# Kernel tuning notes

Hardware: AMD Instinct MI355X
Metric: run time of the kernel (lower is better)

## Reference

```python
import jax, jax.numpy as jnp
import numpy as np

B, Q, K, F, H, D = 2, 4096, 4096, 512, 8, 64

def setup_inputs() -> dict:
    key = jax.random.key(0)
    ks = jax.random.split(key, 6)
    s = 1.0 / np.sqrt(F)
    return {
        "inputs_q": jax.random.normal(ks[0], (B, Q, F), dtype=jnp.float32),
        "inputs_kv": jax.random.normal(ks[1], (B, K, F), dtype=jnp.float32),
        "Wq": jax.random.normal(ks[2], (F, H, D), dtype=jnp.float32) * s,
        "Wk": jax.random.normal(ks[3], (F, H, D), dtype=jnp.float32) * s,
        "Wv": jax.random.normal(ks[4], (F, H, D), dtype=jnp.float32) * s,
        "Wo": jax.random.normal(ks[5], (H, D, F), dtype=jnp.float32) * (1.0 / np.sqrt(H * D)),
    }

def reference(inputs_q, inputs_kv, Wq, Wk, Wv, Wo):
    # QKV projections (DenseGeneral, no bias): [B, L, F] -> [B, L, H, D]
    q = jnp.einsum("bqf,fhd->bqhd", inputs_q, Wq)
    k = jnp.einsum("bkf,fhd->bkhd", inputs_kv, Wk)
    v = jnp.einsum("bkf,fhd->bkhd", inputs_kv, Wv)
    # Explicit attention matrix [B, H, Q, K] as in the original module
    logits = jnp.einsum("bqhd,bkhd->bhqk", q, k)
    attn = jax.nn.softmax(logits, axis=-1)
    out = jnp.einsum("bhqk,bkhd->bqhd", attn, v)
    # Output projection over (heads, head_dim): [B, Q, H, D] -> [B, Q, F]
    return jnp.einsum("bqhd,hdf->bqf", out, Wo)
```

## Files before the change

### kernel.cpp

```cpp
#include <hip/hip_runtime.h>
#include <hip/hip_bf16.h>

typedef short bf16x8 __attribute__((ext_vector_type(8)));
typedef _Float16 f16;
typedef f16 f16x8 __attribute__((ext_vector_type(8)));
typedef float f32x4 __attribute__((ext_vector_type(4)));
typedef unsigned short u16;
typedef u16 u16x8 __attribute__((ext_vector_type(8)));
typedef unsigned int u32;
typedef u32 u32x2 __attribute__((ext_vector_type(2)));

#define B_  2
#define L_  4096
#define F_  512
#define H_  8
#define D_  64
#define M_  8192
#define NSPL 2
#define KHALF (L_ / NSPL)

#define LOG2E 1.442695041f

__device__ inline u16 f2bf(float f) {
    union { float f; unsigned u; } v; v.f = f;
    unsigned r = v.u + 0x7fff + ((v.u >> 16) & 1);
    return (u16)(r >> 16);
}
__device__ inline u16 f2h(float f) {
    union { f16 h; u16 u; } v; v.h = (f16)f;
    return v.u;
}
__device__ inline float h2f(u16 u) {
    union { u16 u; f16 h; } v; v.u = u;
    return (float)v.h;
}

__global__ __launch_bounds__(256) void wt_kernel(
    const float* __restrict__ Wq, const float* __restrict__ Wk,
    const float* __restrict__ Wv, const float* __restrict__ Wo,
    u16* __restrict__ Tq, u16* __restrict__ Tk,
    u16* __restrict__ Tv, u16* __restrict__ To) {
    __shared__ float t[32][33];
    const int z = blockIdx.z;
    const float* in = (z == 0) ? Wq : (z == 1) ? Wk : (z == 2) ? Wv : Wo;
    u16* out = (z == 0) ? Tq : (z == 1) ? Tk : (z == 2) ? Tv : To;
    int k0 = blockIdx.y * 32, n0 = blockIdx.x * 32;
    int c = threadIdx.x & 31, r8 = threadIdx.x >> 5;
#pragma unroll
    for (int i = 0; i < 4; ++i) {
        int r = r8 * 4 + i;
        t[r][c] = in[(size_t)(k0 + r) * F_ + n0 + c];
    }
    __syncthreads();
#pragma unroll
    for (int i = 0; i < 4; ++i) {
        int r = r8 * 4 + i;
        out[(size_t)(n0 + r) * F_ + k0 + c] = f2h(t[c][r]);
    }
}

__global__ __launch_bounds__(256, 3) void proj_kernel(
    const float* __restrict__ Xq, const float* __restrict__ Xkv,
    const u16* __restrict__ Wqt, const u16* __restrict__ Wkt,
    const u16* __restrict__ Wvt,
    u16* __restrict__ Qw, u16* __restrict__ Kw, u16* __restrict__ Vw) {
    __shared__ u16 Ah[128][72];
    __shared__ u16 B1[64][72];
    __shared__ u16 B2[64][72];
    const int tid = threadIdx.x;
    const int w = tid >> 6, lane = tid & 63, lx = lane & 15, quad = lane >> 4;
    const int m0 = blockIdx.y * 128, n0 = blockIdx.x * 64;
    const bool isKV = (blockIdx.z == 1);
    const float* A = isKV ? Xkv : Xq;
    const u16* W1 = isKV ? Wkt : Wqt;

    float4 apre[8];
    u16x8 b1p[2], b2p[2];

    auto load_ab = [&](int k0) {
#pragma unroll
        for (int it = 0; it < 4; ++it) {
            int slot = tid + it * 256, r = slot >> 3, g = (slot & 7) * 8;
            apre[2 * it]     = *(const float4*)(A + (size_t)(m0 + r) * F_ + k0 + g);
            apre[2 * it + 1] = *(const float4*)(A + (size_t)(m0 + r) * F_ + k0 + g + 4);
        }
#pragma unroll
        for (int it = 0; it < 2; ++it) {
            int slot = tid + it * 256, r = slot >> 3, g = (slot & 7) * 8;
            b1p[it] = *(const u16x8*)(W1 + (size_t)(n0 + r) * F_ + k0 + g);
            if (isKV)
                b2p[it] = *(const u16x8*)(Wvt + (size_t)(n0 + r) * F_ + k0 + g);
        }
    };
    auto write_ab = [&]() {
#pragma unroll
        for (int it = 0; it < 4; ++it) {
            int slot = tid + it * 256, r = slot >> 3, g = (slot & 7) * 8;
            float4 f0 = apre[2 * it], f1 = apre[2 * it + 1];
            u16 th[8] = {f2h(f0.x), f2h(f0.y), f2h(f0.z), f2h(f0.w),
                         f2h(f1.x), f2h(f1.y), f2h(f1.z), f2h(f1.w)};
            *(u16x8*)&Ah[r][g] = *(u16x8*)th;
        }
#pragma unroll
        for (int it = 0; it < 2; ++it) {
            int slot = tid + it * 256, r = slot >> 3, g = (slot & 7) * 8;
            *(u16x8*)&B1[r][g] = b1p[it];
            if (isKV) *(u16x8*)&B2[r][g] = b2p[it];
        }
    };

    f32x4 acc1[2][4] = {}, acc2[2][4] = {};

    load_ab(0);
    write_ab();
    __syncthreads();
    load_ab(64);

    for (int k0 = 0; k0 < F_; k0 += 64) {
#pragma unroll
        for (int ks = 0; ks < 2; ++ks) {
            f16x8 af[2];
#pragma unroll
            for (int mf = 0; mf < 2; ++mf)
                af[mf] = *(const f16x8*)&Ah[w * 32 + mf * 16 + lx][ks * 32 + quad * 8];
#pragma unroll
            for (int nt = 0; nt < 4; ++nt) {
                f16x8 b1 = *(const f16x8*)&B1[nt * 16 + lx][ks * 32 + quad * 8];
#pragma unroll
                for (int mf = 0; mf < 2; ++mf)
                    acc1[mf][nt] = __builtin_amdgcn_mfma_f32_16x16x32_f16(af[mf], b1, acc1[mf][nt], 0, 0, 0);
                if (isKV) {
                    f16x8 b2 = *(const f16x8*)&B2[nt * 16 + lx][ks * 32 + quad * 8];
#pragma unroll
                    for (int mf = 0; mf < 2; ++mf)
                        acc2[mf][nt] = __builtin_amdgcn_mfma_f32_16x16x32_f16(af[mf], b2, acc2[mf][nt], 0, 0, 0);
                }
            }
        }
        if (k0 < F_ - 64) {
            __syncthreads();
            write_ab();
            __syncthreads();
            if (k0 < F_ - 128) load_ab(k0 + 128);
        }
    }

    const int h = n0 >> 6;
    const float scl = isKV ? 1.0f : LOG2E;
    u16* C1 = isKV ? Kw : Qw;
#pragma unroll
    for (int mf = 0; mf < 2; ++mf)
#pragma unroll
        for (int nt = 0; nt < 4; ++nt)
#pragma unroll
            for (int i = 0; i < 4; ++i) {
                int m = m0 + w * 32 + mf * 16 + quad * 4 + i;
                int b = m >> 12, l = m & 4095;
                int d = nt * 16 + lx;
                C1[((size_t)(b * H_ + h) * L_ + l) * D_ + d] = f2h(acc1[mf][nt][i] * scl);
            }
    if (isKV) {
        __syncthreads();
#pragma unroll
        for (int mf = 0; mf < 2; ++mf)
#pragma unroll
            for (int nt = 0; nt < 4; ++nt)
#pragma unroll
                for (int i = 0; i < 4; ++i)
                    Ah[w * 32 + mf * 16 + quad * 4 + i][nt * 16 + lx] = f2bf(acc2[mf][nt][i]);
        __syncthreads();
        int d = tid >> 2, seg = (tid & 3) * 32;
        int b = m0 >> 12;
        u16 tmp[32];
#pragma unroll
        for (int j = 0; j < 32; ++j) tmp[j] = Ah[seg + j][d];
        size_t base = ((size_t)(b * H_ + h) * D_ + d) * L_ + (m0 & 4095) + seg;
#pragma unroll
        for (int c = 0; c < 4; ++c)
            *(u16x8*)(Vw + base + c * 8) = *(u16x8*)&tmp[c * 8];
    }
}

__global__ __launch_bounds__(256) void out_gemm(const u16* __restrict__ A16,
                                                const u16* __restrict__ Wt,
                                                float* __restrict__ Cf) {
    __shared__ u16 As[128][72];
    __shared__ u16 Bs[64][72];
    const int tid = threadIdx.x;
    const int w = tid >> 6, lane = tid & 63, lx = lane & 15, quad = lane >> 4;
    const int m0 = blockIdx.y * 128, n0 = blockIdx.x * 64;

    u16x8 a16p[4];
    u16x8 bp[2];

    auto load_ab = [&](int k0) {
#pragma unroll
        for (int it = 0; it < 4; ++it) {
            int slot = tid + it * 256, r = slot >> 3, g = (slot & 7) * 8;
            a16p[it] = *(const u16x8*)(A16 + (size_t)(m0 + r) * F_ + k0 + g);
        }
#pragma unroll
        for (int it = 0; it < 2; ++it) {
            int slot = tid + it * 256, r = slot >> 3, g = (slot & 7) * 8;
            bp[it] = *(const u16x8*)(Wt + (size_t)(n0 + r) * F_ + k0 + g);
        }
    };
    auto write_ab = [&]() {
#pragma unroll
        for (int it = 0; it < 4; ++it) {
            int slot = tid + it * 256, r = slot >> 3, g = (slot & 7) * 8;
            *(u16x8*)&As[r][g] = a16p[it];
        }
#pragma unroll
        for (int it = 0; it < 2; ++it) {
            int slot = tid + it * 256, r = slot >> 3, g = (slot & 7) * 8;
            *(u16x8*)&Bs[r][g] = bp[it];
        }
    };

    f32x4 acc[2][4] = {};

    load_ab(0);
    write_ab();
    __syncthreads();
    load_ab(64);

    for (int k0 = 0; k0 < F_; k0 += 64) {
#pragma unroll
        for (int ks = 0; ks < 2; ++ks) {
            f16x8 af[2];
#pragma unroll
            for (int mf = 0; mf < 2; ++mf)
                af[mf] = *(const f16x8*)&As[w * 32 + mf * 16 + lx][ks * 32 + quad * 8];
#pragma unroll
            for (int nt = 0; nt < 4; ++nt) {
                f16x8 bf = *(const f16x8*)&Bs[nt * 16 + lx][ks * 32 + quad * 8];
#pragma unroll
                for (int mf = 0; mf < 2; ++mf)
                    acc[mf][nt] = __builtin_amdgcn_mfma_f32_16x16x32_f16(af[mf], bf, acc[mf][nt], 0, 0, 0);
            }
        }
        if (k0 < F_ - 64) {
            __syncthreads();
            write_ab();
            __syncthreads();
            if (k0 < F_ - 128) load_ab(k0 + 128);
        }
    }

#pragma unroll
    for (int mf = 0; mf < 2; ++mf)
#pragma unroll
        for (int nt = 0; nt < 4; ++nt)
#pragma unroll
            for (int i = 0; i < 4; ++i) {
                int m = m0 + w * 32 + mf * 16 + quad * 4 + i;
                int n = n0 + nt * 16 + lx;
                Cf[(size_t)m * F_ + n] = acc[mf][nt][i];
            }
}

__global__ __launch_bounds__(256, 4) void flash_mfma(
    const u16* __restrict__ Qg, const u16* __restrict__ Kg,
    const u16* __restrict__ Vtg, u16* __restrict__ On, float* __restrict__ Ls) {
    __shared__ u16 Ks[64][72];
    __shared__ u16 Vs[64][72];

    const int tid = threadIdx.x;
    const int w = tid >> 6, lane = tid & 63, lx = lane & 15, quad = lane >> 4;

    const int x = blockIdx.x;
    const int t = x >> 3;
    const int hh = t >> 6;
    const int s = (t >> 5) & 1;
    const int bh = (x & 7) * 2 + hh;
    const int q0 = (t & 31) * 128;

    const u16* Qp = Qg + ((size_t)bh * L_ + q0) * D_;
    const u16* Kp = Kg + (size_t)bh * L_ * D_ + (size_t)(s * KHALF) * D_;
    const u16* Vp = Vtg + (size_t)bh * D_ * L_ + s * KHALF;

    f16x8 qreg[2][2];
#pragma unroll
    for (int qf = 0; qf < 2; ++qf)
#pragma unroll
        for (int ks = 0; ks < 2; ++ks)
            qreg[qf][ks] = *(const f16x8*)(Qp + (size_t)(w * 32 + qf * 16 + lx) * D_ +
                                           ks * 32 + quad * 8);

    u16x8 kp[2], vp[2];
    auto load_kv = [&](int kt) {
#pragma unroll
        for (int it = 0; it < 2; ++it) {
            int slot = tid + it * 256, r = slot >> 3, g = (slot & 7) * 8;
            kp[it] = *(const u16x8*)(Kp + (size_t)(kt * 64 + r) * D_ + g);
            vp[it] = *(const u16x8*)(Vp + (size_t)r * L_ + kt * 64 + g);
        }
    };
    auto write_kv = [&]() {
#pragma unroll
        for (int it = 0; it < 2; ++it) {
            int slot = tid + it * 256, r = slot >> 3, g = (slot & 7) * 8;
            *(u16x8*)&Ks[r][g] = kp[it];
            *(u16x8*)&Vs[r][g] = vp[it];
        }
    };

    const bf16x8 vone = {0x3F80, 0x3F80, 0x3F80, 0x3F80,
                         0x3F80, 0x3F80, 0x3F80, 0x3F80};
    f32x4 o[2][4] = {};
    f32x4 osum[2] = {};

    load_kv(0);
    write_kv();
    __syncthreads();
    load_kv(1);

    const int NT = KHALF / 64;
    for (int kt = 0; kt < NT; ++kt) {
        f32x4 sv[4][2] = {};
#pragma unroll
        for (int ks = 0; ks < 2; ++ks) {
#pragma unroll
            for (int nt = 0; nt < 4; ++nt) {
                f16x8 ak = *(const f16x8*)&Ks[nt * 16 + lx][ks * 32 + quad * 8];
#pragma unroll
                for (int qf = 0; qf < 2; ++qf)
                    sv[nt][qf] = __builtin_amdgcn_mfma_f32_16x16x32_f16(ak, qreg[qf][ks], sv[nt][qf], 0, 0, 0);
            }
        }

        u32 pu[4][2], pw[4][2];
#pragma unroll
        for (int nt = 0; nt < 4; ++nt)
#pragma unroll
            for (int qf = 0; qf < 2; ++qf) {
                u32 ub[4];
#pragma unroll
                for (int i = 0; i < 4; ++i)
                    ub[i] = __float_as_uint(__builtin_amdgcn_exp2f(sv[nt][qf][i]));
                pu[nt][qf] = __builtin_amdgcn_perm(ub[1], ub[0], 0x07060302u);
                pw[nt][qf] = __builtin_amdgcn_perm(ub[3], ub[2], 0x07060302u);
            }

        bf16x8 ap[2][2];
#pragma unroll
        for (int ks = 0; ks < 2; ++ks)
#pragma unroll
            for (int qf = 0; qf < 2; ++qf) {
                u32x2 r  = __builtin_amdgcn_permlane32_swap(pu[2 * ks][qf], pu[2 * ks + 1][qf], false, false);
                u32x2 r2 = __builtin_amdgcn_permlane16_swap(r[0], r[1], false, false);
                u32x2 t  = __builtin_amdgcn_permlane32_swap(pw[2 * ks][qf], pw[2 * ks + 1][qf], false, false);
                u32x2 t2 = __builtin_amdgcn_permlane16_swap(t[0], t[1], false, false);
                union { u32 d[4]; bf16x8 h; } cvt;
                cvt.d[0] = r2[0];
                cvt.d[1] = t2[0];
                cvt.d[2] = r2[1];
                cvt.d[3] = t2[1];
                ap[ks][qf] = cvt.h;
            }

#pragma unroll
        for (int ks = 0; ks < 2; ++ks) {
#pragma unroll
            for (int qf = 0; qf < 2; ++qf)
                osum[qf] = __builtin_amdgcn_mfma_f32_16x16x32_bf16(ap[ks][qf], vone, osum[qf], 0, 0, 0);
#pragma unroll
            for (int nt = 0; nt < 4; ++nt) {
                bf16x8 bv = *(const bf16x8*)&Vs[nt * 16 + lx][ks * 32 + quad * 8];
#pragma unroll
                for (int qf = 0; qf < 2; ++qf)
                    o[qf][nt] = __builtin_amdgcn_mfma_f32_16x16x32_bf16(ap[ks][qf], bv, o[qf][nt], 0, 0, 0);
            }
        }

        if (kt < NT - 1) {
            __syncthreads();
            write_kv();
            __syncthreads();
            if (kt < NT - 2) load_kv(kt + 2);
        }
    }

    const int b = bh >> 3, h = bh & 7;
    u16* Op = On + (size_t)s * M_ * F_;
#pragma unroll
    for (int qf = 0; qf < 2; ++qf) {
        float linv[4];
#pragma unroll
        for (int i = 0; i < 4; ++i) linv[i] = 1.f / osum[qf][i];
#pragma unroll
        for (int nt = 0; nt < 4; ++nt)
#pragma unroll
            for (int i = 0; i < 4; ++i) {
                int l = q0 + w * 32 + qf * 16 + quad * 4 + i;
                Op[((size_t)b * L_ + l) * (H_ * D_) + h * D_ + nt * 16 + lx] =
                    f2h(o[qf][nt][i] * linv[i]);
            }
        if (lx == 0) {
            float* lp = Ls + ((size_t)s * (B_ * H_) + bh) * L_ +
                        q0 + w * 32 + qf * 16 + quad * 4;
#pragma unroll
            for (int i = 0; i < 4; ++i) lp[i] = osum[qf][i];
        }
    }
}

__global__ __launch_bounds__(256) void reduce_kernel(
    const u16* __restrict__ On, const float* __restrict__ Ls,
    u16* __restrict__ Ow) {
    int gid = blockIdx.x * 256 + threadIdx.x;
    size_t off = (size_t)gid * 8;
    int row = gid >> 3;
    int b = row >> 15, rem = row & 32767;
    int l = rem >> 3, h = rem & 7;
    int lidx = ((b * H_ + h) << 12) + l;
    float l1 = Ls[lidx], l2 = Ls[B_ * H_ * L_ + lidx];
    float w1 = l1 / (l1 + l2), w2 = 1.f - w1;
    u16x8 a = *(const u16x8*)(On + off);
    u16x8 c = *(const u16x8*)(On + (size_t)M_ * F_ + off);
    u16 r[8];
#pragma unroll
    for (int j = 0; j < 8; ++j)
        r[j] = f2h(w1 * h2f(a[j]) + w2 * h2f(c[j]));
    *(u16x8*)(Ow + off) = *(u16x8*)r;
}

extern "C" void kernel_launch(void* const* d_in, const int* in_sizes, int n_in,
                              void* d_out, int out_size, void* d_ws, size_t ws_size,
                              hipStream_t stream)
{
    const float* Xq  = (const float*)d_in[0];
    const float* Xkv = (const float*)d_in[1];
    const float* Wq  = (const float*)d_in[2];
    const float* Wk  = (const float*)d_in[3];
    const float* Wv  = (const float*)d_in[4];
    const float* Wo  = (const float*)d_in[5];
    float* out = (float*)d_out;

    u16* ws  = (u16*)d_ws;
    const size_t MF = (size_t)M_ * F_;
    const size_t FF = (size_t)F_ * F_;
    u16* Wqt = ws;
    u16* Wkt = Wqt + FF;
    u16* Wvt = Wkt + FF;
    u16* Wot = Wvt + FF;
    u16* Qw  = Wot + FF;
    u16* Kw  = Qw + MF;
    u16* Vw  = Kw + MF;
    u16* On  = Vw + MF;
    float* Ls = (float*)(On + 2 * MF);
    u16* Ow  = Qw;

    wt_kernel<<<dim3(16, 16, 4), 256, 0, stream>>>(Wq, Wk, Wv, Wo,
                                                   Wqt, Wkt, Wvt, Wot);

    proj_kernel<<<dim3(8, 64, 2), 256, 0, stream>>>(Xq, Xkv, Wqt, Wkt, Wvt,
                                                    Qw, Kw, Vw);

    flash_mfma<<<dim3(1024), 256, 0, stream>>>(Qw, Kw, Vw, On, Ls);

    reduce_kernel<<<dim3((int)(MF / 8 / 256)), 256, 0, stream>>>(On, Ls, Ow);

    out_gemm<<<dim3(8, 64), 256, 0, stream>>>(Ow, Wot, out);
}
```

Baseline: 232.8 us.

## Double-buffer K/V in LDS, double query tile per block, split key tile into halves

The flash kernel now processes 256 queries per block (64 per wave) so each K/V tile loaded into LDS is reused across twice as many queries, and the grid is halved accordingly. K/V tiles are double-buffered in shared memory, so the next tile is written during compute and only one barrier per iteration remains. The 64-key tile is processed in two 32-key halves so exp/permute work on one half can interleave with MFMAs, with s_setprio raised around the PV MFMA blocks. This raises register and LDS use (launch bounds drop to 2 blocks per CU), trading occupancy for reuse and fewer syncs.

Measured after the change: 215.9 us. 1.08x faster.

```diff
diff --git a/kernel.cpp b/kernel.cpp
--- a/kernel.cpp
+++ b/kernel.cpp
@@ -260,32 +260,32 @@
             }
 }
 
-__global__ __launch_bounds__(256, 4) void flash_mfma(
+__global__ __launch_bounds__(256, 2) void flash_mfma(
     const u16* __restrict__ Qg, const u16* __restrict__ Kg,
     const u16* __restrict__ Vtg, u16* __restrict__ On, float* __restrict__ Ls) {
-    __shared__ u16 Ks[64][72];
-    __shared__ u16 Vs[64][72];
+    __shared__ u16 Ks[2][64][72];
+    __shared__ u16 Vs[2][64][72];
 
     const int tid = threadIdx.x;
     const int w = tid >> 6, lane = tid & 63, lx = lane & 15, quad = lane >> 4;
 
     const int x = blockIdx.x;
     const int t = x >> 3;
-    const int hh = t >> 6;
-    const int s = (t >> 5) & 1;
+    const int hh = t >> 5;
+    const int s = (t >> 4) & 1;
     const int bh = (x & 7) * 2 + hh;
-    const int q0 = (t & 31) * 128;
+    const int q0 = (t & 15) * 256;
 
     const u16* Qp = Qg + ((size_t)bh * L_ + q0) * D_;
     const u16* Kp = Kg + (size_t)bh * L_ * D_ + (size_t)(s * KHALF) * D_;
     const u16* Vp = Vtg + (size_t)bh * D_ * L_ + s * KHALF;
 
-    f16x8 qreg[2][2];
-#pragma unroll
-    for (int qf = 0; qf < 2; ++qf)
+    f16x8 qreg[4][2];
+#pragma unroll
+    for (int qf = 0; qf < 4; ++qf)
 #pragma unroll
         for (int ks = 0; ks < 2; ++ks)
-            qreg[qf][ks] = *(const f16x8*)(Qp + (size_t)(w * 32 + qf * 16 + lx) * D_ +
+            qreg[qf][ks] = *(const f16x8*)(Qp + (size_t)(w * 64 + qf * 16 + lx) * D_ +
                                            ks * 32 + quad * 8);
 
     u16x8 kp[2], vp[2];
@@ -297,95 +297,141 @@
             vp[it] = *(const u16x8*)(Vp + (size_t)r * L_ + kt * 64 + g);
         }
     };
-    auto write_kv = [&]() {
+    auto write_kv = [&](int p) {
 #pragma unroll
         for (int it = 0; it < 2; ++it) {
             int slot = tid + it * 256, r = slot >> 3, g = (slot & 7) * 8;
-            *(u16x8*)&Ks[r][g] = kp[it];
-            *(u16x8*)&Vs[r][g] = vp[it];
+            *(u16x8*)&Ks[p][r][g] = kp[it];
+            *(u16x8*)&Vs[p][r][g] = vp[it];
         }
     };
 
     const bf16x8 vone = {0x3F80, 0x3F80, 0x3F80, 0x3F80,
                          0x3F80, 0x3F80, 0x3F80, 0x3F80};
-    f32x4 o[2][4] = {};
-    f32x4 osum[2] = {};
+    f32x4 o[4][4] = {};
+    f32x4 osum[4] = {};
 
     load_kv(0);
-    write_kv();
+    write_kv(0);
     __syncthreads();
     load_kv(1);
 
     const int NT = KHALF / 64;
     for (int kt = 0; kt < NT; ++kt) {
-        f32x4 sv[4][2] = {};
-#pragma unroll
-        for (int ks = 0; ks < 2; ++ks) {
-#pragma unroll
-            for (int nt = 0; nt < 4; ++nt) {
-                f16x8 ak = *(const f16x8*)&Ks[nt * 16 + lx][ks * 32 + quad * 8];
-#pragma unroll
-                for (int qf = 0; qf < 2; ++qf)
+        const int p = kt & 1;
+
+        f32x4 sv[2][4] = {};
+#pragma unroll
+        for (int ks = 0; ks < 2; ++ks)
+#pragma unroll
+            for (int nt = 0; nt < 2; ++nt) {
+                f16x8 ak = *(const f16x8*)&Ks[p][nt * 16 + lx][ks * 32 + quad * 8];
+#pragma unroll
+                for (int qf = 0; qf < 4; ++qf)
                     sv[nt][qf] = __builtin_amdgcn_mfma_f32_16x16x32_f16(ak, qreg[qf][ks], sv[nt][qf], 0, 0, 0);
             }
-        }
-
-        u32 pu[4][2], pw[4][2];
-#pragma unroll
-        for (int nt = 0; nt < 4; ++nt)
-#pragma unroll
-            for (int qf = 0; qf < 2; ++qf) {
+
+        if (kt < NT - 1) write_kv(p ^ 1);
+
+        bf16x8 ap0[4];
+#pragma unroll
+        for (int qf = 0; qf < 4; ++qf) {
+            u32 pu[2], pw[2];
+#pragma unroll
+            for (int nt = 0; nt < 2; ++nt) {
                 u32 ub[4];
 #pragma unroll
                 for (int i = 0; i < 4; ++i)
                     ub[i] = __float_as_uint(__builtin_amdgcn_exp2f(sv[nt][qf][i]));
-                pu[nt][qf] = __builtin_amdgcn_perm(ub[1], ub[0], 0x07060302u);
-                pw[nt][qf] = __builtin_amdgcn_perm(ub[3], ub[2], 0x07060302u);
-            }
-
-        bf16x8 ap[2][2];
+                pu[nt] = __builtin_amdgcn_perm(ub[1], ub[0], 0x07060302u);
+                pw[nt] = __builtin_amdgcn_perm(ub[3], ub[2], 0x07060302u);
+            }
+            u32x2 r  = __builtin_amdgcn_permlane32_swap(pu[0], pu[1], false, false);
+            u32x2 r2 = __builtin_amdgcn_permlane16_swap(r[0], r[1], false, false);
+            u32x2 tt = __builtin_amdgcn_permlane32_swap(pw[0], pw[1], false, false);
+            u32x2 t2 = __builtin_amdgcn_permlane16_swap(tt[0], tt[1], false, false);
+            union { u32 d[4]; bf16x8 h; } cvt;
+            cvt.d[0] = r2[0];
+            cvt.d[1] = t2[0];
+            cvt.d[2] = r2[1];
+            cvt.d[3] = t2[1];
+            ap0[qf] = cvt.h;
+        }
+
+        __builtin_amdgcn_s_setprio(1);
+#pragma unroll
+        for (int qf = 0; qf < 4; ++qf)
+            osum[qf] = __builtin_amdgcn_mfma_f32_16x16x32_bf16(ap0[qf], vone, osum[qf], 0, 0, 0);
+#pragma unroll
+        for (int nt = 0; nt < 4; ++nt) {
+            bf16x8 bv = *(const bf16x8*)&Vs[p][nt * 16 + lx][quad * 8];
+#pragma unroll
+            for (int qf = 0; qf < 4; ++qf)
+                o[qf][nt] = __builtin_amdgcn_mfma_f32_16x16x32_bf16(ap0[qf], bv, o[qf][nt], 0, 0, 0);
+        }
+        __builtin_amdgcn_s_setprio(0);
+
+#pragma unroll
+        for (int nt = 0; nt < 2; ++nt)
+#pragma unroll
+            for (int qf = 0; qf < 4; ++qf)
+                sv[nt][qf] = (f32x4){0.f, 0.f, 0.f, 0.f};
 #pragma unroll
         for (int ks = 0; ks < 2; ++ks)
 #pragma unroll
-            for (int qf = 0; qf < 2; ++qf) {
-                u32x2 r  = __builtin_amdgcn_permlane32_swap(pu[2 * ks][qf], pu[2 * ks + 1][qf], false, false);
-                u32x2 r2 = __builtin_amdgcn_permlane16_swap(r[0], r[1], false, false);
-                u32x2 t  = __builtin_amdgcn_permlane32_swap(pw[2 * ks][qf], pw[2 * ks + 1][qf], false, false);
-                u32x2 t2 = __builtin_amdgcn_permlane16_swap(t[0], t[1], false, false);
-                union { u32 d[4]; bf16x8 h; } cvt;
-                cvt.d[0] = r2[0];
-                cvt.d[1] = t2[0];
-                cvt.d[2] = r2[1];
-                cvt.d[3] = t2[1];
-                ap[ks][qf] = cvt.h;
-            }
-
-#pragma unroll
-        for (int ks = 0; ks < 2; ++ks) {
-#pragma unroll
-            for (int qf = 0; qf < 2; ++qf)
-                osum[qf] = __builtin_amdgcn_mfma_f32_16x16x32_bf16(ap[ks][qf], vone, osum[qf], 0, 0, 0);
-#pragma unroll
-            for (int nt = 0; nt < 4; ++nt) {
-                bf16x8 bv = *(const bf16x8*)&Vs[nt * 16 + lx][ks * 32 + quad * 8];
-#pragma unroll
-                for (int qf = 0; qf < 2; ++qf)
-                    o[qf][nt] = __builtin_amdgcn_mfma_f32_16x16x32_bf16(ap[ks][qf], bv, o[qf][nt], 0, 0, 0);
-            }
-        }
-
-        if (kt < NT - 1) {
-            __syncthreads();
-            write_kv();
-            __syncthreads();
-            if (kt < NT - 2) load_kv(kt + 2);
-        }
+            for (int nt = 0; nt < 2; ++nt) {
+                f16x8 ak = *(const f16x8*)&Ks[p][(nt + 2) * 16 + lx][ks * 32 + quad * 8];
+#pragma unroll
+                for (int qf = 0; qf < 4; ++qf)
+                    sv[nt][qf] = __builtin_amdgcn_mfma_f32_16x16x32_f16(ak, qreg[qf][ks], sv[nt][qf], 0, 0, 0);
+            }
+
+        bf16x8 ap1[4];
+#pragma unroll
+        for (int qf = 0; qf < 4; ++qf) {
+            u32 pu[2], pw[2];
+#pragma unroll
+            for (int nt = 0; nt < 2; ++nt) {
+                u32 ub[4];
+#pragma unroll
+                for (int i = 0; i < 4; ++i)
+                    ub[i] = __float_as_uint(__builtin_amdgcn_exp2f(sv[nt][qf][i]));
+                pu[nt] = __builtin_amdgcn_perm(ub[1], ub[0], 0x07060302u);
+                pw[nt] = __builtin_amdgcn_perm(ub[3], ub[2], 0x07060302u);
+            }
+            u32x2 r  = __builtin_amdgcn_permlane32_swap(pu[0], pu[1], false, false);
+            u32x2 r2 = __builtin_amdgcn_permlane16_swap(r[0], r[1], false, false);
+            u32x2 tt = __builtin_amdgcn_permlane32_swap(pw[0], pw[1], false, false);
+            u32x2 t2 = __builtin_amdgcn_permlane16_swap(tt[0], tt[1], false, false);
+            union { u32 d[4]; bf16x8 h; } cvt;
+            cvt.d[0] = r2[0];
+            cvt.d[1] = t2[0];
+            cvt.d[2] = r2[1];
+            cvt.d[3] = t2[1];
+            ap1[qf] = cvt.h;
+        }
+
+        __builtin_amdgcn_s_setprio(1);
+#pragma unroll
+        for (int qf = 0; qf < 4; ++qf)
+            osum[qf] = __builtin_amdgcn_mfma_f32_16x16x32_bf16(ap1[qf], vone, osum[qf], 0, 0, 0);
+#pragma unroll
+        for (int nt = 0; nt < 4; ++nt) {
+            bf16x8 bv = *(const bf16x8*)&Vs[p][nt * 16 + lx][32 + quad * 8];
+#pragma unroll
+            for (int qf = 0; qf < 4; ++qf)
+                o[qf][nt] = __builtin_amdgcn_mfma_f32_16x16x32_bf16(ap1[qf], bv, o[qf][nt], 0, 0, 0);
+        }
+        __builtin_amdgcn_s_setprio(0);
+
+        if (kt < NT - 2) load_kv(kt + 2);
+        if (kt < NT - 1) __syncthreads();
     }
 
     const int b = bh >> 3, h = bh & 7;
     u16* Op = On + (size_t)s * M_ * F_;
 #pragma unroll
-    for (int qf = 0; qf < 2; ++qf) {
+    for (int qf = 0; qf < 4; ++qf) {
         float linv[4];
 #pragma unroll
         for (int i = 0; i < 4; ++i) linv[i] = 1.f / osum[qf][i];
@@ -393,13 +439,13 @@
         for (int nt = 0; nt < 4; ++nt)
 #pragma unroll
             for (int i = 0; i < 4; ++i) {
-                int l = q0 + w * 32 + qf * 16 + quad * 4 + i;
+                int l = q0 + w * 64 + qf * 16 + quad * 4 + i;
                 Op[((size_t)b * L_ + l) * (H_ * D_) + h * D_ + nt * 16 + lx] =
                     f2h(o[qf][nt][i] * linv[i]);
             }
         if (lx == 0) {
             float* lp = Ls + ((size_t)s * (B_ * H_) + bh) * L_ +
-                        q0 + w * 32 + qf * 16 + quad * 4;
+                        q0 + w * 64 + qf * 16 + quad * 4;
 #pragma unroll
             for (int i = 0; i < 4; ++i) lp[i] = osum[qf][i];
         }
@@ -458,7 +504,7 @@
     proj_kernel<<<dim3(8, 64, 2), 256, 0, stream>>>(Xq, Xkv, Wqt, Wkt, Wvt,
                                                     Qw, Kw, Vw);
 
-    flash_mfma<<<dim3(1024), 256, 0, stream>>>(Qw, Kw, Vw, On, Ls);
+    flash_mfma<<<dim3(512), 256, 0, stream>>>(Qw, Kw, Vw, On, Ls);
 
     reduce_kernel<<<dim3((int)(MF / 8 / 256)), 256, 0, stream>>>(On, Ls, Ow);
 
```
